# Kernel tuning notes

Hardware: AMD Instinct MI355X
Metric: run time of the kernel (lower is better)

Reference implementation:

```python
import jax, jax.numpy as jnp
import numpy as np

N, E = 50000, 1600000
C_IN, C_H, C_OUT = 36, 64, 64
EPS = 1e-16  # PyG softmax denominator epsilon


def setup_inputs() -> dict:
    key = jax.random.key(0)
    ks = jax.random.split(key, 48)
    inp = {}
    inp["features"] = jax.random.normal(ks[0], (N, C_IN), dtype=jnp.float32)
    inp["edge_attr"] = jax.random.uniform(ks[1], (E, 1), dtype=jnp.float32)
    inp["edge_index"] = jax.random.randint(ks[2], (2, E), 0, N, dtype=jnp.int32)
    dims = [(C_IN, C_H), (C_H, C_H), (C_H, C_H), (C_H, C_OUT)]
    i = 3
    for l, (din, dout) in enumerate(dims, 1):
        s = 1.0 / np.sqrt(din)
        inp[f"Wl{l}"] = jax.random.normal(ks[i], (din, dout), jnp.float32) * s; i += 1
        inp[f"bl{l}"] = jax.random.normal(ks[i], (dout,), jnp.float32) * 0.02; i += 1
        inp[f"Wr{l}"] = jax.random.normal(ks[i], (din, dout), jnp.float32) * s; i += 1
        inp[f"br{l}"] = jax.random.normal(ks[i], (dout,), jnp.float32) * 0.02; i += 1
        inp[f"We{l}"] = jax.random.normal(ks[i], (1, dout), jnp.float32); i += 1
        inp[f"att{l}"] = jax.random.normal(ks[i], (dout,), jnp.float32) * s; i += 1
        inp[f"bo{l}"] = jax.random.normal(ks[i], (dout,), jnp.float32) * 0.02; i += 1
    mlp = [(C_OUT, C_OUT // 2, "m1"), (C_OUT // 2, C_OUT // 4, "m2"), (C_OUT // 4, 1, "m3")]
    for din, dout, tag in mlp:
        s = 1.0 / np.sqrt(din)
        inp[f"W{tag}"] = jax.random.normal(ks[i], (din, dout), jnp.float32) * s; i += 1
        inp[f"b{tag}"] = jax.random.normal(ks[i], (dout,), jnp.float32) * 0.02; i += 1
    return inp


def gatv2_conv(x, src, dst, edge_attr, Wl, bl, Wr, br, We, att, bo):
    """Single-head GATv2Conv with edge features (PyG semantics)."""
    xl = x @ Wl + bl                      # [N, dout] source transform
    xr = x @ Wr + br                      # [N, dout] target transform
    ea = edge_attr @ We                   # [E, dout]
    e = jax.nn.leaky_relu(xl[src] + xr[dst] + ea, 0.2)  # [E, dout]
    score = e @ att                       # [E]
    # segment softmax over edges sharing a destination node
    m = jax.ops.segment_max(score, dst, num_segments=N)
    a = jnp.exp(score - m[dst])
    denom = jax.ops.segment_sum(a, dst, num_segments=N)
    alpha = a / (denom[dst] + EPS)
    out = jax.ops.segment_sum(xl[src] * alpha[:, None], dst, num_segments=N)
    return out + bo


def reference(features, edge_attr, edge_index,
              Wl1, bl1, Wr1, br1, We1, att1, bo1,
              Wl2, bl2, Wr2, br2, We2, att2, bo2,
              Wl3, bl3, Wr3, br3, We3, att3, bo3,
              Wl4, bl4, Wr4, br4, We4, att4, bo4,
              Wm1, bm1, Wm2, bm2, Wm3, bm3):
    src, dst = edge_index[0], edge_index[1]
    x = jax.nn.relu(gatv2_conv(features, src, dst, edge_attr, Wl1, bl1, Wr1, br1, We1, att1, bo1))
    x = jax.nn.relu(gatv2_conv(x, src, dst, edge_attr, Wl2, bl2, Wr2, br2, We2, att2, bo2))
    x = jax.nn.relu(gatv2_conv(x, src, dst, edge_attr, Wl3, bl3, Wr3, br3, We3, att3, bo3))
    x = jax.nn.relu(gatv2_conv(x, src, dst, edge_attr, Wl4, bl4, Wr4, br4, We4, att4, bo4))
    x = jnp.mean(x, axis=-2)              # graph readout -> [C_OUT]
    x = jax.nn.relu(x @ Wm1 + bm1)
    x = jax.nn.relu(x @ Wm2 + bm2)
    return x @ Wm3 + bm3                  # [1]
```

## Files before the change

kernel.cpp:

```cpp
#include <hip/hip_runtime.h>


__device__ __forceinline__ int rfl(int v) { return __builtin_amdgcn_readfirstlane(v); }

#define NBK_MAX 256
#define BCAP 9216

__global__ void __launch_bounds__(256) k_build1(
    const int* __restrict__ src, const int* __restrict__ dst,
    const float* __restrict__ ea_in, int* __restrict__ bcur,
    uint2* __restrict__ tmp, int E, int nbk, int SG,
    const float* __restrict__ x, const float* __restrict__ Wl,
    const float* __restrict__ bl, const float* __restrict__ Wr,
    const float* __restrict__ br, float* __restrict__ xl,
    float* __restrict__ xr, int nNodes) {
  __shared__ __align__(16) float smem[6976];
  int tid = threadIdx.x;
  if ((int)blockIdx.x < SG) {
    int* cnt = (int*)smem;
    int* cur = cnt + 256;
    int* gb  = cur + 256;
    if (tid < nbk) { cnt[tid] = 0; cur[tid] = 0; }
    __syncthreads();
    int base = blockIdx.x * 2048 + tid;
    uint2 rec[8];
    #pragma unroll
    for (int k = 0; k < 8; k++) {
      int e = base + k * 256;
      if (e < E) {
        unsigned d = (unsigned)dst[e];
        rec[k] = make_uint2((d << 16) | (unsigned)src[e],
                            (unsigned)__float_as_int(ea_in[e]));
        atomicAdd(&cnt[d >> 8], 1);
      } else {
        rec[k] = make_uint2(0u, 0u);
      }
    }
    __syncthreads();
    if (tid < nbk) {
      int c = cnt[tid];
      gb[tid] = (c > 0) ? atomicAdd(&bcur[tid * 16], c) : 0;
    }
    __syncthreads();
    #pragma unroll
    for (int k = 0; k < 8; k++) {
      int e = base + k * 256;
      if (e < E) {
        int b = (int)(rec[k].x >> 24);
        int slot = atomicAdd(&cur[b], 1);
        tmp[(size_t)b * BCAP + gb[b] + slot] = rec[k];
      }
    }
  } else {
    const int DIN = 36;
    float* sWl = smem;
    float* sWr = smem + 2304;
    float (*sx)[DIN + 1] = (float(*)[DIN + 1])(smem + 4608);
    for (int i = tid; i < DIN * 64; i += 256) { sWl[i] = Wl[i]; sWr[i] = Wr[i]; }
    int nb = ((int)blockIdx.x - SG) * 64;
    for (int i = tid; i < 64 * DIN; i += 256) {
      int ln = i / DIN, c = i % DIN;
      int g = nb + ln;
      sx[ln][c] = (g < nNodes) ? x[(size_t)g * DIN + c] : 0.f;
    }
    __syncthreads();
    int c4 = (tid & 15) * 4;
    int ns = (tid >> 4) * 4;
    float4 bl4 = *(const float4*)(bl + c4);
    float4 br4 = *(const float4*)(br + c4);
    float4 L0 = bl4, L1 = bl4, L2 = bl4, L3 = bl4;
    float4 R0 = br4, R1 = br4, R2 = br4, R3 = br4;
    const float* x0 = sx[ns + 0];
    const float* x1 = sx[ns + 1];
    const float* x2 = sx[ns + 2];
    const float* x3 = sx[ns + 3];
    #pragma unroll 4
    for (int k = 0; k < DIN; k++) {
      float4 wl = *(const float4*)(sWl + k * 64 + c4);
      float4 wr = *(const float4*)(sWr + k * 64 + c4);
      float a = x0[k], bb = x1[k], c = x2[k], dd = x3[k];
      L0.x = fmaf(a, wl.x, L0.x);  L0.y = fmaf(a, wl.y, L0.y);
      L0.z = fmaf(a, wl.z, L0.z);  L0.w = fmaf(a, wl.w, L0.w);
      R0.x = fmaf(a, wr.x, R0.x);  R0.y = fmaf(a, wr.y, R0.y);
      R0.z = fmaf(a, wr.z, R0.z);  R0.w = fmaf(a, wr.w, R0.w);
      L1.x = fmaf(bb, wl.x, L1.x); L1.y = fmaf(bb, wl.y, L1.y);
      L1.z = fmaf(bb, wl.z, L1.z); L1.w = fmaf(bb, wl.w, L1.w);
      R1.x = fmaf(bb, wr.x, R1.x); R1.y = fmaf(bb, wr.y, R1.y);
      R1.z = fmaf(bb, wr.z, R1.z); R1.w = fmaf(bb, wr.w, R1.w);
      L2.x = fmaf(c, wl.x, L2.x);  L2.y = fmaf(c, wl.y, L2.y);
      L2.z = fmaf(c, wl.z, L2.z);  L2.w = fmaf(c, wl.w, L2.w);
      R2.x = fmaf(c, wr.x, R2.x);  R2.y = fmaf(c, wr.y, R2.y);
      R2.z = fmaf(c, wr.z, R2.z);  R2.w = fmaf(c, wr.w, R2.w);
      L3.x = fmaf(dd, wl.x, L3.x); L3.y = fmaf(dd, wl.y, L3.y);
      L3.z = fmaf(dd, wl.z, L3.z); L3.w = fmaf(dd, wl.w, L3.w);
      R3.x = fmaf(dd, wr.x, R3.x); R3.y = fmaf(dd, wr.y, R3.y);
      R3.z = fmaf(dd, wr.z, R3.z); R3.w = fmaf(dd, wr.w, R3.w);
    }
    int g = nb + ns;
    if (g + 0 < nNodes) { *(float4*)(xl + (size_t)(g+0)*64 + c4) = L0; *(float4*)(xr + (size_t)(g+0)*64 + c4) = R0; }
    if (g + 1 < nNodes) { *(float4*)(xl + (size_t)(g+1)*64 + c4) = L1; *(float4*)(xr + (size_t)(g+1)*64 + c4) = R1; }
    if (g + 2 < nNodes) { *(float4*)(xl + (size_t)(g+2)*64 + c4) = L2; *(float4*)(xr + (size_t)(g+2)*64 + c4) = R2; }
    if (g + 3 < nNodes) { *(float4*)(xl + (size_t)(g+3)*64 + c4) = L3; *(float4*)(xr + (size_t)(g+3)*64 + c4) = R3; }
  }
}

__global__ void __launch_bounds__(1024) k_csr(const int* __restrict__ bcur,
                                              const uint2* __restrict__ tmp,
                                              int2* __restrict__ pairs,
                                              int* __restrict__ rowptr,
                                              int N, int nbk) {
  __shared__ int cnt[256];
  __shared__ int pref[256];
  __shared__ int cur[256];
  __shared__ int wsum[16];
  __shared__ int lo_s;
  int b = blockIdx.x;
  int n0 = b << 8;
  int tid = threadIdx.x, lane = tid & 63, wv = tid >> 6;
  if (tid < 256) { cnt[tid] = 0; cur[tid] = 0; }
  int contrib = (tid < nbk && tid < b) ? bcur[tid * 16] : 0;
  #pragma unroll
  for (int o = 32; o > 0; o >>= 1) contrib += __shfl_xor(contrib, o, 64);
  if (lane == 0) wsum[wv] = contrib;
  __syncthreads();
  if (tid == 0) {
    int s = 0;
    for (int i = 0; i < 16; i++) s += wsum[i];
    lo_s = s;
  }
  __syncthreads();
  int lo = lo_s;
  int cb = bcur[b * 16];
  const uint2* tb = tmp + (size_t)b * BCAP;
  for (int k = tid; k < cb; k += 1024)
    atomicAdd(&cnt[(int)(tb[k].x >> 16) - n0], 1);
  __syncthreads();
  int v = 0, x = 0;
  if (tid < 256) {
    v = cnt[tid];
    x = v;
    #pragma unroll
    for (int o = 1; o < 64; o <<= 1) {
      int t = __shfl_up(x, o, 64);
      if (lane >= o) x += t;
    }
    if (lane == 63) wsum[wv] = x;
  }
  __syncthreads();
  if (tid < 256) {
    int wo = 0;
    for (int k = 0; k < 4; k++) if (k < wv) wo += wsum[k];
    int start = lo + wo + (x - v);
    pref[tid] = start;
    int nn = n0 + tid;
    if (nn <= N) rowptr[nn] = start;
  }
  __syncthreads();
  for (int k = tid; k < cb; k += 1024) {
    uint2 rec = tb[k];
    int local = (int)(rec.x >> 16) - n0;
    int pos = pref[local] + atomicAdd(&cur[local], 1);
    pairs[pos] = make_int2((int)(rec.x & 0xffffu), (int)rec.y);
  }
}

template <int DIN>
__global__ void __launch_bounds__(256) k_transform(
    const float* __restrict__ x, const float* __restrict__ Wl, const float* __restrict__ bl,
    const float* __restrict__ Wr, const float* __restrict__ br,
    float* __restrict__ xl, float* __restrict__ xr, int nNodes) {
  __shared__ __align__(16) float sWl[DIN * 64];
  __shared__ __align__(16) float sWr[DIN * 64];
  __shared__ float sx[64][DIN + 1];
  int tid = threadIdx.x;
  for (int i = tid; i < DIN * 64; i += 256) { sWl[i] = Wl[i]; sWr[i] = Wr[i]; }
  int nb = blockIdx.x * 64;
  for (int i = tid; i < 64 * DIN; i += 256) {
    int ln = i / DIN, c = i % DIN;
    int g = nb + ln;
    sx[ln][c] = (g < nNodes) ? x[(size_t)g * DIN + c] : 0.f;
  }
  __syncthreads();
  int c4 = (tid & 15) * 4;
  int ns = (tid >> 4) * 4;
  float4 bl4 = *(const float4*)(bl + c4);
  float4 br4 = *(const float4*)(br + c4);
  float4 L0 = bl4, L1 = bl4, L2 = bl4, L3 = bl4;
  float4 R0 = br4, R1 = br4, R2 = br4, R3 = br4;
  const float* x0 = sx[ns + 0];
  const float* x1 = sx[ns + 1];
  const float* x2 = sx[ns + 2];
  const float* x3 = sx[ns + 3];
  #pragma unroll 4
  for (int k = 0; k < DIN; k++) {
    float4 wl = *(const float4*)(sWl + k * 64 + c4);
    float4 wr = *(const float4*)(sWr + k * 64 + c4);
    float a = x0[k], bb = x1[k], c = x2[k], dd = x3[k];
    L0.x = fmaf(a, wl.x, L0.x);  L0.y = fmaf(a, wl.y, L0.y);
    L0.z = fmaf(a, wl.z, L0.z);  L0.w = fmaf(a, wl.w, L0.w);
    R0.x = fmaf(a, wr.x, R0.x);  R0.y = fmaf(a, wr.y, R0.y);
    R0.z = fmaf(a, wr.z, R0.z);  R0.w = fmaf(a, wr.w, R0.w);
    L1.x = fmaf(bb, wl.x, L1.x); L1.y = fmaf(bb, wl.y, L1.y);
    L1.z = fmaf(bb, wl.z, L1.z); L1.w = fmaf(bb, wl.w, L1.w);
    R1.x = fmaf(bb, wr.x, R1.x); R1.y = fmaf(bb, wr.y, R1.y);
    R1.z = fmaf(bb, wr.z, R1.z); R1.w = fmaf(bb, wr.w, R1.w);
    L2.x = fmaf(c, wl.x, L2.x);  L2.y = fmaf(c, wl.y, L2.y);
    L2.z = fmaf(c, wl.z, L2.z);  L2.w = fmaf(c, wl.w, L2.w);
    R2.x = fmaf(c, wr.x, R2.x);  R2.y = fmaf(c, wr.y, R2.y);
    R2.z = fmaf(c, wr.z, R2.z);  R2.w = fmaf(c, wr.w, R2.w);
    L3.x = fmaf(dd, wl.x, L3.x); L3.y = fmaf(dd, wl.y, L3.y);
    L3.z = fmaf(dd, wl.z, L3.z); L3.w = fmaf(dd, wl.w, L3.w);
    R3.x = fmaf(dd, wr.x, R3.x); R3.y = fmaf(dd, wr.y, R3.y);
    R3.z = fmaf(dd, wr.z, R3.z); R3.w = fmaf(dd, wr.w, R3.w);
  }
  int g = nb + ns;
  if (g + 0 < nNodes) { *(float4*)(xl + (size_t)(g+0)*64 + c4) = L0; *(float4*)(xr + (size_t)(g+0)*64 + c4) = R0; }
  if (g + 1 < nNodes) { *(float4*)(xl + (size_t)(g+1)*64 + c4) = L1; *(float4*)(xr + (size_t)(g+1)*64 + c4) = R1; }
  if (g + 2 < nNodes) { *(float4*)(xl + (size_t)(g+2)*64 + c4) = L2; *(float4*)(xr + (size_t)(g+2)*64 + c4) = R2; }
  if (g + 3 < nNodes) { *(float4*)(xl + (size_t)(g+3)*64 + c4) = L3; *(float4*)(xr + (size_t)(g+3)*64 + c4) = R3; }
}

#define SC1(T, EA, OUT) { float u, acc; \
  u = T.x + fmaf(EA, We4.x, xr4.x); u = fmaxf(u, 0.2f * u); acc = at4.x * u; \
  u = T.y + fmaf(EA, We4.y, xr4.y); u = fmaxf(u, 0.2f * u); acc = fmaf(at4.y, u, acc); \
  u = T.z + fmaf(EA, We4.z, xr4.z); u = fmaxf(u, 0.2f * u); acc = fmaf(at4.z, u, acc); \
  u = T.w + fmaf(EA, We4.w, xr4.w); u = fmaxf(u, 0.2f * u); acc = fmaf(at4.w, u, acc); \
  OUT = acc; }

__global__ void __launch_bounds__(256, 5) k_edge(
    const float* __restrict__ xl, const float* __restrict__ xr,
    const int* __restrict__ rowptr, const int2* __restrict__ pairs,
    const float* __restrict__ We, const float* __restrict__ att,
    const float* __restrict__ bo, float* __restrict__ xout, int nNodes) {
  int lane = threadIdx.x & 63;
  int wv = rfl((int)(threadIdx.x >> 6));
  int n = rfl(blockIdx.x * 4 + wv);
  if (n >= nNodes) return;
  int c4 = lane & 15;
  int r  = lane >> 4;
  int cb = c4 * 4;

  float4 We4 = *(const float4*)(We + cb);
  float4 at4 = *(const float4*)(att + cb);
  float4 xr4 = *(const float4*)(xr + (size_t)n * 64 + cb);
  int s0 = rfl(rowptr[n]);
  int s1 = rfl(rowptr[n + 1]);
  int last = s1 - 1;

  float m = -3.0e38f, d = 0.f;
  float4 A = {0.f, 0.f, 0.f, 0.f};

  for (int kb = s0; kb < s1; kb += 16) {
    int cnt = rfl(min(16, s1 - kb));
    int2 p0 = pairs[min(kb + r,      last)];
    int2 p1 = pairs[min(kb + 4 + r,  last)];
    int2 p2 = pairs[min(kb + 8 + r,  last)];
    int2 p3 = pairs[min(kb + 12 + r, last)];
    float ea0 = __int_as_float(p0.y);
    float ea1 = __int_as_float(p1.y);
    float ea2 = __int_as_float(p2.y);
    float ea3 = __int_as_float(p3.y);

    float4 t0 = *(const float4*)(xl + (size_t)(unsigned)p0.x * 64 + cb);
    float4 t1 = *(const float4*)(xl + (size_t)(unsigned)p1.x * 64 + cb);
    float4 t2 = *(const float4*)(xl + (size_t)(unsigned)p2.x * 64 + cb);
    float4 t3 = *(const float4*)(xl + (size_t)(unsigned)p3.x * 64 + cb);

    float sc0, sc1, sc2, sc3;
    SC1(t0, ea0, sc0)
    SC1(t1, ea1, sc1)
    SC1(t2, ea2, sc2)
    SC1(t3, ea3, sc3)

    #pragma unroll
    for (int o = 1; o <= 8; o <<= 1) {
      sc0 += __shfl_xor(sc0, o, 64);
      sc1 += __shfl_xor(sc1, o, 64);
      sc2 += __shfl_xor(sc2, o, 64);
      sc3 += __shfl_xor(sc3, o, 64);
    }
    sc0 = (r < cnt)      ? sc0 : -3.0e38f;
    sc1 = (4 + r < cnt)  ? sc1 : -3.0e38f;
    sc2 = (8 + r < cnt)  ? sc2 : -3.0e38f;
    sc3 = (12 + r < cnt) ? sc3 : -3.0e38f;

    float mc = fmaxf(fmaxf(sc0, sc1), fmaxf(sc2, sc3));
    mc = fmaxf(mc, __shfl_xor(mc, 16, 64));
    mc = fmaxf(mc, __shfl_xor(mc, 32, 64));
    float newm = fmaxf(m, mc);
    float rf = __expf(m - newm);
    float a0 = __expf(sc0 - newm);
    float a1 = __expf(sc1 - newm);
    float a2 = __expf(sc2 - newm);
    float a3 = __expf(sc3 - newm);
    float ds = (a0 + a1) + (a2 + a3);
    ds += __shfl_xor(ds, 16, 64);
    ds += __shfl_xor(ds, 32, 64);
    d = d * rf + ds;
    m = newm;

    A.x = fmaf(a0, t0.x, A.x * rf); A.y = fmaf(a0, t0.y, A.y * rf);
    A.z = fmaf(a0, t0.z, A.z * rf); A.w = fmaf(a0, t0.w, A.w * rf);
    A.x = fmaf(a1, t1.x, A.x); A.y = fmaf(a1, t1.y, A.y);
    A.z = fmaf(a1, t1.z, A.z); A.w = fmaf(a1, t1.w, A.w);
    A.x = fmaf(a2, t2.x, A.x); A.y = fmaf(a2, t2.y, A.y);
    A.z = fmaf(a2, t2.z, A.z); A.w = fmaf(a2, t2.w, A.w);
    A.x = fmaf(a3, t3.x, A.x); A.y = fmaf(a3, t3.y, A.y);
    A.z = fmaf(a3, t3.z, A.z); A.w = fmaf(a3, t3.w, A.w);
  }

  A.x += __shfl_xor(A.x, 16, 64); A.y += __shfl_xor(A.y, 16, 64);
  A.z += __shfl_xor(A.z, 16, 64); A.w += __shfl_xor(A.w, 16, 64);
  A.x += __shfl_xor(A.x, 32, 64); A.y += __shfl_xor(A.y, 32, 64);
  A.z += __shfl_xor(A.z, 32, 64); A.w += __shfl_xor(A.w, 32, 64);

  float inv = 1.f / (d + 1e-16f);
  if (r == 0) {
    float4 bo4 = *(const float4*)(bo + cb);
    float4 o4;
    o4.x = fmaxf(fmaf(A.x, inv, bo4.x), 0.f);
    o4.y = fmaxf(fmaf(A.y, inv, bo4.y), 0.f);
    o4.z = fmaxf(fmaf(A.z, inv, bo4.z), 0.f);
    o4.w = fmaxf(fmaf(A.w, inv, bo4.w), 0.f);
    *(float4*)(xout + (size_t)n * 64 + cb) = o4;
  }
}

__global__ void k_mean(const float* __restrict__ x, double* __restrict__ meanbuf, int nNodes) {
  __shared__ float sacc[256];
  int lane = threadIdx.x & 63;
  int wv = threadIdx.x >> 6;
  int gw = blockIdx.x * 4 + wv;
  int stride = gridDim.x * 4;
  float acc = 0.f;
  for (int n = gw; n < nNodes; n += stride) acc += x[(size_t)n * 64 + lane];
  sacc[threadIdx.x] = acc;
  __syncthreads();
  if (threadIdx.x < 64) {
    float a = sacc[threadIdx.x] + sacc[threadIdx.x + 64] + sacc[threadIdx.x + 128] + sacc[threadIdx.x + 192];
    atomicAdd(&meanbuf[lane], (double)a);
  }
}

__global__ void k_mlp(const double* __restrict__ meanbuf,
                      const float* __restrict__ Wm1, const float* __restrict__ bm1,
                      const float* __restrict__ Wm2, const float* __restrict__ bm2,
                      const float* __restrict__ Wm3, const float* __restrict__ bm3,
                      float* __restrict__ out, double invN) {
  __shared__ float xm[64];
  __shared__ float h1[32];
  __shared__ float h2[16];
  int t = threadIdx.x;
  xm[t] = (float)(meanbuf[t] * invN);
  __syncthreads();
  if (t < 32) {
    float a = bm1[t];
    for (int c = 0; c < 64; c++) a = fmaf(xm[c], Wm1[c * 32 + t], a);
    h1[t] = fmaxf(a, 0.f);
  }
  __syncthreads();
  if (t < 16) {
    float a = bm2[t];
    for (int c = 0; c < 32; c++) a = fmaf(h1[c], Wm2[c * 16 + t], a);
    h2[t] = fmaxf(a, 0.f);
  }
  __syncthreads();
  if (t == 0) {
    float a = bm3[0];
    for (int c = 0; c < 16; c++) a = fmaf(h2[c], Wm3[c], a);
    out[0] = a;
  }
}

extern "C" void kernel_launch(void* const* d_in, const int* in_sizes, int n_in,
                              void* d_out, int out_size, void* d_ws, size_t ws_size,
                              hipStream_t stream) {
  (void)n_in; (void)out_size; (void)ws_size;
  const int N = in_sizes[0] / 36;
  const int E = in_sizes[1];

  const float* feat = (const float*)d_in[0];
  const float* eat  = (const float*)d_in[1];
  const int*   eidx = (const int*)d_in[2];
  const int* src = eidx;
  const int* dst = eidx + E;

  const float* L[4][7];
  for (int l = 0; l < 4; l++)
    for (int j = 0; j < 7; j++) L[l][j] = (const float*)d_in[3 + l * 7 + j];
  const float* Wm1 = (const float*)d_in[31];
  const float* bm1 = (const float*)d_in[32];
  const float* Wm2 = (const float*)d_in[33];
  const float* bm2 = (const float*)d_in[34];
  const float* Wm3 = (const float*)d_in[35];
  const float* bm3 = (const float*)d_in[36];

  const int NBK = (N + 255) >> 8;

  char* ws = (char*)d_ws;
  size_t off = 0;
  auto alloc = [&](size_t bytes) {
    off = (off + 511) & ~(size_t)511;
    void* p = ws + off;
    off += bytes;
    return p;
  };
  int*    bcur    = (int*)alloc((size_t)NBK * 16 * 4);
  double* meanbuf = (double*)alloc(64 * 8);
  size_t zero_bytes = off;
  int*    rowptr  = (int*)alloc((size_t)(N + 1) * 4);
  int2*   pairs   = (int2*)alloc((size_t)E * 8);
  float*  xA      = (float*)alloc((size_t)N * 64 * 4);
  float*  xB      = (float*)alloc((size_t)N * 64 * 4);
  uint2*  tmp     = (uint2*)alloc((size_t)NBK * BCAP * 8);
  float*  xC      = (float*)tmp;

  hipMemsetAsync(d_ws, 0, zero_bytes, stream);

  int SG = (E + 2047) / 2048;
  int TG = (N + 63) / 64;
  int tgrid = TG;
  int ngrid = (N + 3) / 4;

  k_build1<<<SG + TG, 256, 0, stream>>>(src, dst, eat, bcur, tmp, E, NBK, SG,
                                        feat, L[0][0], L[0][1], L[0][2], L[0][3],
                                        xA, xB, N);
  k_csr<<<NBK, 1024, 0, stream>>>(bcur, tmp, pairs, rowptr, N, NBK);
  k_edge<<<ngrid, 256, 0, stream>>>(xA, xB, rowptr, pairs,
                                    L[0][4], L[0][5], L[0][6], xC, N);

  for (int l = 1; l < 4; l++) {
    k_transform<64><<<tgrid, 256, 0, stream>>>(xC, L[l][0], L[l][1], L[l][2], L[l][3], xA, xB, N);
    k_edge<<<ngrid, 256, 0, stream>>>(xA, xB, rowptr, pairs,
                                      L[l][4], L[l][5], L[l][6], xC, N);
  }

  k_mean<<<256, 256, 0, stream>>>(xC, meanbuf, N);
  k_mlp<<<1, 64, 0, stream>>>(meanbuf, Wm1, bm1, Wm2, bm2, Wm3, bm3, (float*)d_out, 1.0 / (double)N);
}
```

Measured before the change: 490.4 us.

## Process four nodes per wave with prefetched edge pairs and pre-scaled source offsets

Each wave in the edge kernel now handles four consecutive destination nodes instead of one, reusing the rowptr boundary and the loaded bias. It prefetches the next 16 edge pairs while the current batch is processed, so the min-clamp against the last edge is dropped and the pairs buffer is padded with zeroed entries. Source indices are stored pre-multiplied by 64, so the gather address becomes a simple OR. The online-softmax rescale is now applied only when the max grows. The cost is fewer waves in the grid, which reduces parallelism and latency hiding, and the work is serialized across the four nodes.

```diff
diff --git a/kernel.cpp b/kernel.cpp
--- a/kernel.cpp
+++ b/kernel.cpp
@@ -160,7 +160,7 @@
     uint2 rec = tb[k];
     int local = (int)(rec.x >> 16) - n0;
     int pos = pref[local] + atomicAdd(&cur[local], 1);
-    pairs[pos] = make_int2((int)(rec.x & 0xffffu), (int)rec.y);
+    pairs[pos] = make_int2((int)((rec.x & 0xffffu) << 6), (int)rec.y);
   }
 }
 
@@ -234,95 +234,112 @@
     const float* __restrict__ bo, float* __restrict__ xout, int nNodes) {
   int lane = threadIdx.x & 63;
   int wv = rfl((int)(threadIdx.x >> 6));
-  int n = rfl(blockIdx.x * 4 + wv);
-  if (n >= nNodes) return;
+  int nbase = rfl(((int)blockIdx.x * 4 + wv) * 4);
+  if (nbase >= nNodes) return;
   int c4 = lane & 15;
   int r  = lane >> 4;
   int cb = c4 * 4;
 
   float4 We4 = *(const float4*)(We + cb);
   float4 at4 = *(const float4*)(att + cb);
-  float4 xr4 = *(const float4*)(xr + (size_t)n * 64 + cb);
-  int s0 = rfl(rowptr[n]);
-  int s1 = rfl(rowptr[n + 1]);
-  int last = s1 - 1;
-
-  float m = -3.0e38f, d = 0.f;
-  float4 A = {0.f, 0.f, 0.f, 0.f};
-
-  for (int kb = s0; kb < s1; kb += 16) {
-    int cnt = rfl(min(16, s1 - kb));
-    int2 p0 = pairs[min(kb + r,      last)];
-    int2 p1 = pairs[min(kb + 4 + r,  last)];
-    int2 p2 = pairs[min(kb + 8 + r,  last)];
-    int2 p3 = pairs[min(kb + 12 + r, last)];
-    float ea0 = __int_as_float(p0.y);
-    float ea1 = __int_as_float(p1.y);
-    float ea2 = __int_as_float(p2.y);
-    float ea3 = __int_as_float(p3.y);
-
-    float4 t0 = *(const float4*)(xl + (size_t)(unsigned)p0.x * 64 + cb);
-    float4 t1 = *(const float4*)(xl + (size_t)(unsigned)p1.x * 64 + cb);
-    float4 t2 = *(const float4*)(xl + (size_t)(unsigned)p2.x * 64 + cb);
-    float4 t3 = *(const float4*)(xl + (size_t)(unsigned)p3.x * 64 + cb);
-
-    float sc0, sc1, sc2, sc3;
-    SC1(t0, ea0, sc0)
-    SC1(t1, ea1, sc1)
-    SC1(t2, ea2, sc2)
-    SC1(t3, ea3, sc3)
-
-    #pragma unroll
-    for (int o = 1; o <= 8; o <<= 1) {
-      sc0 += __shfl_xor(sc0, o, 64);
-      sc1 += __shfl_xor(sc1, o, 64);
-      sc2 += __shfl_xor(sc2, o, 64);
-      sc3 += __shfl_xor(sc3, o, 64);
-    }
-    sc0 = (r < cnt)      ? sc0 : -3.0e38f;
-    sc1 = (4 + r < cnt)  ? sc1 : -3.0e38f;
-    sc2 = (8 + r < cnt)  ? sc2 : -3.0e38f;
-    sc3 = (12 + r < cnt) ? sc3 : -3.0e38f;
-
-    float mc = fmaxf(fmaxf(sc0, sc1), fmaxf(sc2, sc3));
-    mc = fmaxf(mc, __shfl_xor(mc, 16, 64));
-    mc = fmaxf(mc, __shfl_xor(mc, 32, 64));
-    float newm = fmaxf(m, mc);
-    float rf = __expf(m - newm);
-    float a0 = __expf(sc0 - newm);
-    float a1 = __expf(sc1 - newm);
-    float a2 = __expf(sc2 - newm);
-    float a3 = __expf(sc3 - newm);
-    float ds = (a0 + a1) + (a2 + a3);
-    ds += __shfl_xor(ds, 16, 64);
-    ds += __shfl_xor(ds, 32, 64);
-    d = d * rf + ds;
-    m = newm;
-
-    A.x = fmaf(a0, t0.x, A.x * rf); A.y = fmaf(a0, t0.y, A.y * rf);
-    A.z = fmaf(a0, t0.z, A.z * rf); A.w = fmaf(a0, t0.w, A.w * rf);
-    A.x = fmaf(a1, t1.x, A.x); A.y = fmaf(a1, t1.y, A.y);
-    A.z = fmaf(a1, t1.z, A.z); A.w = fmaf(a1, t1.w, A.w);
-    A.x = fmaf(a2, t2.x, A.x); A.y = fmaf(a2, t2.y, A.y);
-    A.z = fmaf(a2, t2.z, A.z); A.w = fmaf(a2, t2.w, A.w);
-    A.x = fmaf(a3, t3.x, A.x); A.y = fmaf(a3, t3.y, A.y);
-    A.z = fmaf(a3, t3.z, A.z); A.w = fmaf(a3, t3.w, A.w);
-  }
-
-  A.x += __shfl_xor(A.x, 16, 64); A.y += __shfl_xor(A.y, 16, 64);
-  A.z += __shfl_xor(A.z, 16, 64); A.w += __shfl_xor(A.w, 16, 64);
-  A.x += __shfl_xor(A.x, 32, 64); A.y += __shfl_xor(A.y, 32, 64);
-  A.z += __shfl_xor(A.z, 32, 64); A.w += __shfl_xor(A.w, 32, 64);
-
-  float inv = 1.f / (d + 1e-16f);
-  if (r == 0) {
-    float4 bo4 = *(const float4*)(bo + cb);
-    float4 o4;
-    o4.x = fmaxf(fmaf(A.x, inv, bo4.x), 0.f);
-    o4.y = fmaxf(fmaf(A.y, inv, bo4.y), 0.f);
-    o4.z = fmaxf(fmaf(A.z, inv, bo4.z), 0.f);
-    o4.w = fmaxf(fmaf(A.w, inv, bo4.w), 0.f);
-    *(float4*)(xout + (size_t)n * 64 + cb) = o4;
+  float4 bo4 = *(const float4*)(bo + cb);
+
+  int nend = min(nbase + 4, nNodes);
+  int s1 = rfl(rowptr[nbase]);
+  for (int n = nbase; n < nend; n++) {
+    int s0 = s1;
+    s1 = rfl(rowptr[n + 1]);
+    float4 xr4 = *(const float4*)(xr + (size_t)n * 64 + cb);
+
+    float m = -3.0e38f, d = 0.f;
+    float4 A = {0.f, 0.f, 0.f, 0.f};
+
+    int kb = s0;
+    int2 q0 = pairs[kb + r];
+    int2 q1 = pairs[kb + 4 + r];
+    int2 q2 = pairs[kb + 8 + r];
+    int2 q3 = pairs[kb + 12 + r];
+
+    while (kb < s1) {
+      int2 p0 = q0, p1 = q1, p2 = q2, p3 = q3;
+      int cnt = rfl(min(16, s1 - kb));
+      kb += 16;
+      q0 = pairs[kb + r];
+      q1 = pairs[kb + 4 + r];
+      q2 = pairs[kb + 8 + r];
+      q3 = pairs[kb + 12 + r];
+
+      float ea0 = __int_as_float(p0.y);
+      float ea1 = __int_as_float(p1.y);
+      float ea2 = __int_as_float(p2.y);
+      float ea3 = __int_as_float(p3.y);
+
+      float4 t0 = *(const float4*)(xl + (unsigned)(p0.x | cb));
+      float4 t1 = *(const float4*)(xl + (unsigned)(p1.x | cb));
+      float4 t2 = *(const float4*)(xl + (unsigned)(p2.x | cb));
+      float4 t3 = *(const float4*)(xl + (unsigned)(p3.x | cb));
+
+      float sc0, sc1, sc2, sc3;
+      SC1(t0, ea0, sc0)
+      SC1(t1, ea1, sc1)
+      SC1(t2, ea2, sc2)
+      SC1(t3, ea3, sc3)
+
+      #pragma unroll
+      for (int o = 1; o <= 8; o <<= 1) {
+        sc0 += __shfl_xor(sc0, o, 64);
+        sc1 += __shfl_xor(sc1, o, 64);
+        sc2 += __shfl_xor(sc2, o, 64);
+        sc3 += __shfl_xor(sc3, o, 64);
+      }
+      sc0 = (r < cnt)      ? sc0 : -3.0e38f;
+      sc1 = (4 + r < cnt)  ? sc1 : -3.0e38f;
+      sc2 = (8 + r < cnt)  ? sc2 : -3.0e38f;
+      sc3 = (12 + r < cnt) ? sc3 : -3.0e38f;
+
+      float mc = fmaxf(fmaxf(sc0, sc1), fmaxf(sc2, sc3));
+      mc = fmaxf(mc, __shfl_xor(mc, 16, 64));
+      mc = fmaxf(mc, __shfl_xor(mc, 32, 64));
+      float newm = fmaxf(m, mc);
+      if (newm > m) {
+        float rf = __expf(m - newm);
+        d *= rf;
+        A.x *= rf; A.y *= rf; A.z *= rf; A.w *= rf;
+        m = newm;
+      }
+      float a0 = __expf(sc0 - m);
+      float a1 = __expf(sc1 - m);
+      float a2 = __expf(sc2 - m);
+      float a3 = __expf(sc3 - m);
+      float ds = (a0 + a1) + (a2 + a3);
+      ds += __shfl_xor(ds, 16, 64);
+      ds += __shfl_xor(ds, 32, 64);
+      d += ds;
+
+      A.x = fmaf(a0, t0.x, A.x); A.y = fmaf(a0, t0.y, A.y);
+      A.z = fmaf(a0, t0.z, A.z); A.w = fmaf(a0, t0.w, A.w);
+      A.x = fmaf(a1, t1.x, A.x); A.y = fmaf(a1, t1.y, A.y);
+      A.z = fmaf(a1, t1.z, A.z); A.w = fmaf(a1, t1.w, A.w);
+      A.x = fmaf(a2, t2.x, A.x); A.y = fmaf(a2, t2.y, A.y);
+      A.z = fmaf(a2, t2.z, A.z); A.w = fmaf(a2, t2.w, A.w);
+      A.x = fmaf(a3, t3.x, A.x); A.y = fmaf(a3, t3.y, A.y);
+      A.z = fmaf(a3, t3.z, A.z); A.w = fmaf(a3, t3.w, A.w);
+    }
+
+    A.x += __shfl_xor(A.x, 16, 64); A.y += __shfl_xor(A.y, 16, 64);
+    A.z += __shfl_xor(A.z, 16, 64); A.w += __shfl_xor(A.w, 16, 64);
+    A.x += __shfl_xor(A.x, 32, 64); A.y += __shfl_xor(A.y, 32, 64);
+    A.z += __shfl_xor(A.z, 32, 64); A.w += __shfl_xor(A.w, 32, 64);
+
+    float inv = 1.f / (d + 1e-16f);
+    if (r == 0) {
+      float4 o4;
+      o4.x = fmaxf(fmaf(A.x, inv, bo4.x), 0.f);
+      o4.y = fmaxf(fmaf(A.y, inv, bo4.y), 0.f);
+      o4.z = fmaxf(fmaf(A.z, inv, bo4.z), 0.f);
+      o4.w = fmaxf(fmaf(A.w, inv, bo4.w), 0.f);
+      *(float4*)(xout + (size_t)n * 64 + cb) = o4;
+    }
   }
 }
 
@@ -409,18 +426,19 @@
   double* meanbuf = (double*)alloc(64 * 8);
   size_t zero_bytes = off;
   int*    rowptr  = (int*)alloc((size_t)(N + 1) * 4);
-  int2*   pairs   = (int2*)alloc((size_t)E * 8);
+  int2*   pairs   = (int2*)alloc((size_t)(E + 32) * 8);
   float*  xA      = (float*)alloc((size_t)N * 64 * 4);
   float*  xB      = (float*)alloc((size_t)N * 64 * 4);
   uint2*  tmp     = (uint2*)alloc((size_t)NBK * BCAP * 8);
   float*  xC      = (float*)tmp;
 
   hipMemsetAsync(d_ws, 0, zero_bytes, stream);
+  hipMemsetAsync(pairs + E, 0, 32 * sizeof(int2), stream);
 
   int SG = (E + 2047) / 2048;
   int TG = (N + 63) / 64;
   int tgrid = TG;
-  int ngrid = (N + 3) / 4;
+  int ngrid = (N + 15) / 16;
 
   k_build1<<<SG + TG, 256, 0, stream>>>(src, dst, eat, bcur, tmp, E, NBK, SG,
                                         feat, L[0][0], L[0][1], L[0][2], L[0][3],
```

New measurement: 519.8 us. +6.0%, slower.

## Rework edge kernel to 8-channel lanes with premultiplied source offsets

Applied to the files above, without the earlier changes.

Each lane in the edge aggregation kernel now handles 8 channels across 8 edge rows instead of 4 channels across 4 rows, giving fewer shuffle reduction steps per edge batch. The CSR build stores source indices already multiplied by 64 so the gather address is a single OR. The bounds clamp on pair reads is dropped in favour of a zero-padded tail in the pairs buffer. The online-softmax rescale now runs only when the running max increases. The cost is more registers per lane and a divergent branch around the rescale.

```diff
diff --git a/kernel.cpp b/kernel.cpp
--- a/kernel.cpp
+++ b/kernel.cpp
@@ -160,7 +160,7 @@
     uint2 rec = tb[k];
     int local = (int)(rec.x >> 16) - n0;
     int pos = pref[local] + atomicAdd(&cur[local], 1);
-    pairs[pos] = make_int2((int)(rec.x & 0xffffu), (int)rec.y);
+    pairs[pos] = make_int2((int)((rec.x & 0xffffu) << 6), (int)rec.y);
   }
 }
 
@@ -220,11 +220,15 @@
   if (g + 3 < nNodes) { *(float4*)(xl + (size_t)(g+3)*64 + c4) = L3; *(float4*)(xr + (size_t)(g+3)*64 + c4) = R3; }
 }
 
-#define SC1(T, EA, OUT) { float u, acc; \
-  u = T.x + fmaf(EA, We4.x, xr4.x); u = fmaxf(u, 0.2f * u); acc = at4.x * u; \
-  u = T.y + fmaf(EA, We4.y, xr4.y); u = fmaxf(u, 0.2f * u); acc = fmaf(at4.y, u, acc); \
-  u = T.z + fmaf(EA, We4.z, xr4.z); u = fmaxf(u, 0.2f * u); acc = fmaf(at4.z, u, acc); \
-  u = T.w + fmaf(EA, We4.w, xr4.w); u = fmaxf(u, 0.2f * u); acc = fmaf(at4.w, u, acc); \
+#define SC8(TA, TB, EA, OUT) { float u, acc; \
+  u = TA.x + fmaf(EA, Wea.x, xra.x); u = fmaxf(u, 0.2f * u); acc = ata.x * u; \
+  u = TA.y + fmaf(EA, Wea.y, xra.y); u = fmaxf(u, 0.2f * u); acc = fmaf(ata.y, u, acc); \
+  u = TA.z + fmaf(EA, Wea.z, xra.z); u = fmaxf(u, 0.2f * u); acc = fmaf(ata.z, u, acc); \
+  u = TA.w + fmaf(EA, Wea.w, xra.w); u = fmaxf(u, 0.2f * u); acc = fmaf(ata.w, u, acc); \
+  u = TB.x + fmaf(EA, Web.x, xrb.x); u = fmaxf(u, 0.2f * u); acc = fmaf(atb.x, u, acc); \
+  u = TB.y + fmaf(EA, Web.y, xrb.y); u = fmaxf(u, 0.2f * u); acc = fmaf(atb.y, u, acc); \
+  u = TB.z + fmaf(EA, Web.z, xrb.z); u = fmaxf(u, 0.2f * u); acc = fmaf(atb.z, u, acc); \
+  u = TB.w + fmaf(EA, Web.w, xrb.w); u = fmaxf(u, 0.2f * u); acc = fmaf(atb.w, u, acc); \
   OUT = acc; }
 
 __global__ void __launch_bounds__(256, 5) k_edge(
@@ -236,93 +240,104 @@
   int wv = rfl((int)(threadIdx.x >> 6));
   int n = rfl(blockIdx.x * 4 + wv);
   if (n >= nNodes) return;
-  int c4 = lane & 15;
-  int r  = lane >> 4;
-  int cb = c4 * 4;
-
-  float4 We4 = *(const float4*)(We + cb);
-  float4 at4 = *(const float4*)(att + cb);
-  float4 xr4 = *(const float4*)(xr + (size_t)n * 64 + cb);
+  int c8 = lane & 7;
+  int r  = lane >> 3;
+  int cb = c8 * 8;
+
+  float4 Wea = *(const float4*)(We + cb);
+  float4 Web = *(const float4*)(We + cb + 4);
+  float4 ata = *(const float4*)(att + cb);
+  float4 atb = *(const float4*)(att + cb + 4);
+  const float* xrp = xr + (size_t)n * 64 + cb;
+  float4 xra = *(const float4*)(xrp);
+  float4 xrb = *(const float4*)(xrp + 4);
   int s0 = rfl(rowptr[n]);
   int s1 = rfl(rowptr[n + 1]);
-  int last = s1 - 1;
 
   float m = -3.0e38f, d = 0.f;
-  float4 A = {0.f, 0.f, 0.f, 0.f};
+  float4 Aa = {0.f, 0.f, 0.f, 0.f};
+  float4 Ab = {0.f, 0.f, 0.f, 0.f};
 
   for (int kb = s0; kb < s1; kb += 16) {
     int cnt = rfl(min(16, s1 - kb));
-    int2 p0 = pairs[min(kb + r,      last)];
-    int2 p1 = pairs[min(kb + 4 + r,  last)];
-    int2 p2 = pairs[min(kb + 8 + r,  last)];
-    int2 p3 = pairs[min(kb + 12 + r, last)];
+    int2 p0 = pairs[kb + r];
+    int2 p1 = pairs[kb + 8 + r];
     float ea0 = __int_as_float(p0.y);
     float ea1 = __int_as_float(p1.y);
-    float ea2 = __int_as_float(p2.y);
-    float ea3 = __int_as_float(p3.y);
-
-    float4 t0 = *(const float4*)(xl + (size_t)(unsigned)p0.x * 64 + cb);
-    float4 t1 = *(const float4*)(xl + (size_t)(unsigned)p1.x * 64 + cb);
-    float4 t2 = *(const float4*)(xl + (size_t)(unsigned)p2.x * 64 + cb);
-    float4 t3 = *(const float4*)(xl + (size_t)(unsigned)p3.x * 64 + cb);
-
-    float sc0, sc1, sc2, sc3;
-    SC1(t0, ea0, sc0)
-    SC1(t1, ea1, sc1)
-    SC1(t2, ea2, sc2)
-    SC1(t3, ea3, sc3)
+
+    const float* r0 = xl + (unsigned)(p0.x | cb);
+    const float* r1 = xl + (unsigned)(p1.x | cb);
+    float4 t0a = *(const float4*)(r0);
+    float4 t0b = *(const float4*)(r0 + 4);
+    float4 t1a = *(const float4*)(r1);
+    float4 t1b = *(const float4*)(r1 + 4);
+
+    float sc0, sc1;
+    SC8(t0a, t0b, ea0, sc0)
+    SC8(t1a, t1b, ea1, sc1)
 
     #pragma unroll
-    for (int o = 1; o <= 8; o <<= 1) {
+    for (int o = 1; o <= 4; o <<= 1) {
       sc0 += __shfl_xor(sc0, o, 64);
       sc1 += __shfl_xor(sc1, o, 64);
-      sc2 += __shfl_xor(sc2, o, 64);
-      sc3 += __shfl_xor(sc3, o, 64);
-    }
-    sc0 = (r < cnt)      ? sc0 : -3.0e38f;
-    sc1 = (4 + r < cnt)  ? sc1 : -3.0e38f;
-    sc2 = (8 + r < cnt)  ? sc2 : -3.0e38f;
-    sc3 = (12 + r < cnt) ? sc3 : -3.0e38f;
-
-    float mc = fmaxf(fmaxf(sc0, sc1), fmaxf(sc2, sc3));
+    }
+    sc0 = (r < cnt)     ? sc0 : -3.0e38f;
+    sc1 = (8 + r < cnt) ? sc1 : -3.0e38f;
+
+    float mc = fmaxf(sc0, sc1);
+    mc = fmaxf(mc, __shfl_xor(mc, 8, 64));
     mc = fmaxf(mc, __shfl_xor(mc, 16, 64));
     mc = fmaxf(mc, __shfl_xor(mc, 32, 64));
     float newm = fmaxf(m, mc);
-    float rf = __expf(m - newm);
-    float a0 = __expf(sc0 - newm);
-    float a1 = __expf(sc1 - newm);
-    float a2 = __expf(sc2 - newm);
-    float a3 = __expf(sc3 - newm);
-    float ds = (a0 + a1) + (a2 + a3);
+    if (newm > m) {
+      float rf = __expf(m - newm);
+      d *= rf;
+      Aa.x *= rf; Aa.y *= rf; Aa.z *= rf; Aa.w *= rf;
+      Ab.x *= rf; Ab.y *= rf; Ab.z *= rf; Ab.w *= rf;
+      m = newm;
+    }
+    float a0 = __expf(sc0 - m);
+    float a1 = __expf(sc1 - m);
+    float ds = a0 + a1;
+    ds += __shfl_xor(ds, 8, 64);
     ds += __shfl_xor(ds, 16, 64);
     ds += __shfl_xor(ds, 32, 64);
-    d = d * rf + ds;
-    m = newm;
-
-    A.x = fmaf(a0, t0.x, A.x * rf); A.y = fmaf(a0, t0.y, A.y * rf);
-    A.z = fmaf(a0, t0.z, A.z * rf); A.w = fmaf(a0, t0.w, A.w * rf);
-    A.x = fmaf(a1, t1.x, A.x); A.y = fmaf(a1, t1.y, A.y);
-    A.z = fmaf(a1, t1.z, A.z); A.w = fmaf(a1, t1.w, A.w);
-    A.x = fmaf(a2, t2.x, A.x); A.y = fmaf(a2, t2.y, A.y);
-    A.z = fmaf(a2, t2.z, A.z); A.w = fmaf(a2, t2.w, A.w);
-    A.x = fmaf(a3, t3.x, A.x); A.y = fmaf(a3, t3.y, A.y);
-    A.z = fmaf(a3, t3.z, A.z); A.w = fmaf(a3, t3.w, A.w);
-  }
-
-  A.x += __shfl_xor(A.x, 16, 64); A.y += __shfl_xor(A.y, 16, 64);
-  A.z += __shfl_xor(A.z, 16, 64); A.w += __shfl_xor(A.w, 16, 64);
-  A.x += __shfl_xor(A.x, 32, 64); A.y += __shfl_xor(A.y, 32, 64);
-  A.z += __shfl_xor(A.z, 32, 64); A.w += __shfl_xor(A.w, 32, 64);
+    d += ds;
+
+    Aa.x = fmaf(a0, t0a.x, Aa.x); Aa.y = fmaf(a0, t0a.y, Aa.y);
+    Aa.z = fmaf(a0, t0a.z, Aa.z); Aa.w = fmaf(a0, t0a.w, Aa.w);
+    Ab.x = fmaf(a0, t0b.x, Ab.x); Ab.y = fmaf(a0, t0b.y, Ab.y);
+    Ab.z = fmaf(a0, t0b.z, Ab.z); Ab.w = fmaf(a0, t0b.w, Ab.w);
+    Aa.x = fmaf(a1, t1a.x, Aa.x); Aa.y = fmaf(a1, t1a.y, Aa.y);
+    Aa.z = fmaf(a1, t1a.z, Aa.z); Aa.w = fmaf(a1, t1a.w, Aa.w);
+    Ab.x = fmaf(a1, t1b.x, Ab.x); Ab.y = fmaf(a1, t1b.y, Ab.y);
+    Ab.z = fmaf(a1, t1b.z, Ab.z); Ab.w = fmaf(a1, t1b.w, Ab.w);
+  }
+
+  #pragma unroll
+  for (int o = 8; o <= 32; o <<= 1) {
+    Aa.x += __shfl_xor(Aa.x, o, 64); Aa.y += __shfl_xor(Aa.y, o, 64);
+    Aa.z += __shfl_xor(Aa.z, o, 64); Aa.w += __shfl_xor(Aa.w, o, 64);
+    Ab.x += __shfl_xor(Ab.x, o, 64); Ab.y += __shfl_xor(Ab.y, o, 64);
+    Ab.z += __shfl_xor(Ab.z, o, 64); Ab.w += __shfl_xor(Ab.w, o, 64);
+  }
 
   float inv = 1.f / (d + 1e-16f);
   if (r == 0) {
-    float4 bo4 = *(const float4*)(bo + cb);
-    float4 o4;
-    o4.x = fmaxf(fmaf(A.x, inv, bo4.x), 0.f);
-    o4.y = fmaxf(fmaf(A.y, inv, bo4.y), 0.f);
-    o4.z = fmaxf(fmaf(A.z, inv, bo4.z), 0.f);
-    o4.w = fmaxf(fmaf(A.w, inv, bo4.w), 0.f);
-    *(float4*)(xout + (size_t)n * 64 + cb) = o4;
+    float4 boa = *(const float4*)(bo + cb);
+    float4 bob = *(const float4*)(bo + cb + 4);
+    float4 oa, ob;
+    oa.x = fmaxf(fmaf(Aa.x, inv, boa.x), 0.f);
+    oa.y = fmaxf(fmaf(Aa.y, inv, boa.y), 0.f);
+    oa.z = fmaxf(fmaf(Aa.z, inv, boa.z), 0.f);
+    oa.w = fmaxf(fmaf(Aa.w, inv, boa.w), 0.f);
+    ob.x = fmaxf(fmaf(Ab.x, inv, bob.x), 0.f);
+    ob.y = fmaxf(fmaf(Ab.y, inv, bob.y), 0.f);
+    ob.z = fmaxf(fmaf(Ab.z, inv, bob.z), 0.f);
+    ob.w = fmaxf(fmaf(Ab.w, inv, bob.w), 0.f);
+    float* op = xout + (size_t)n * 64 + cb;
+    *(float4*)(op) = oa;
+    *(float4*)(op + 4) = ob;
   }
 }
 
@@ -409,13 +424,14 @@
   double* meanbuf = (double*)alloc(64 * 8);
   size_t zero_bytes = off;
   int*    rowptr  = (int*)alloc((size_t)(N + 1) * 4);
-  int2*   pairs   = (int2*)alloc((size_t)E * 8);
+  int2*   pairs   = (int2*)alloc((size_t)(E + 32) * 8);
   float*  xA      = (float*)alloc((size_t)N * 64 * 4);
   float*  xB      = (float*)alloc((size_t)N * 64 * 4);
   uint2*  tmp     = (uint2*)alloc((size_t)NBK * BCAP * 8);
   float*  xC      = (float*)tmp;
 
   hipMemsetAsync(d_ws, 0, zero_bytes, stream);
+  hipMemsetAsync(pairs + E, 0, 32 * sizeof(int2), stream);
 
   int SG = (E + 2047) / 2048;
   int TG = (N + 63) / 64;
```

New measurement: 538.2 us. 1.1x slower.
